# Kernel optimization log

Measured on AMD Instinct MI355X. Metric: run time of the kernel, lower is better.

## Reference

```python
import jax, jax.numpy as jnp
import numpy as np

EPS = 1e-7
K = 15      # kernel_size
CIN = 128
F = 256


def setup_inputs() -> dict:
    key = jax.random.key(0)
    k1, k2 = jax.random.split(key)
    x = jax.random.normal(k1, (32, 4096, CIN), dtype=jnp.float32)
    # glorot-uniform init then UnitNorm over axes (0,1) per filter, matching the constraint
    limit = np.sqrt(6.0 / (K * CIN + F))
    kernel = jax.random.uniform(k2, (K, CIN, F), dtype=jnp.float32, minval=-limit, maxval=limit)
    kernel = kernel / jnp.sqrt(jnp.sum(kernel * kernel, axis=(0, 1), keepdims=True) + 1e-12)
    scale = jnp.full((1, 1, 1), 10.0, dtype=jnp.float32)
    bias = jnp.zeros((F,), dtype=jnp.float32)
    return {"inputs": x, "kernel": kernel, "scale": scale, "bias": bias}


def reference(inputs, kernel, scale, bias):
    # dot-product conv: (B, L-K+1, F), VALID padding, stride 1
    dot = jax.lax.conv_general_dilated(
        inputs, kernel, window_strides=(1,), padding="VALID",
        dimension_numbers=("NWC", "WIO", "NWC"))
    # sliding sum-of-squares over window*channels. In the original this is a
    # conv1d with an all-ones (K,CIN,F) kernel, i.e. every filter sees the same
    # scalar sum -> compute it once via a cumsum box filter and broadcast.
    k = kernel.shape[0]
    sq = jnp.sum(inputs * inputs, axis=-1)                       # (B, L)
    cs = jnp.cumsum(jnp.pad(sq, ((0, 0), (1, 0))), axis=1)       # (B, L+1)
    win = cs[:, k:] - cs[:, :-k]                                 # (B, L-K+1)
    norm_x = jnp.sqrt(win + EPS)[..., None]                      # (B, L-K+1, 1)
    return scale * (dot / norm_x) + bias
```

## Files before the change

kernel.cpp:

```cpp
#include <hip/hip_runtime.h>
#include <hip/hip_bf16.h>
#include <stdint.h>

#define K_TAPS 15
#define CIN    128
#define F_OUT  256
#define LSEQ   4096
#define LOUT   (LSEQ - K_TAPS + 1)
#define BATCH  32

typedef __attribute__((ext_vector_type(8))) short bf16x8;
typedef __attribute__((ext_vector_type(4))) float f32x4;

typedef __attribute__((address_space(1))) const unsigned int gu32_t;
typedef __attribute__((address_space(3))) unsigned int su32_t;

__global__ void prep_w_kernel(const float* __restrict__ W,
                              unsigned short* __restrict__ Wp) {
  int idx = blockIdx.x * 256 + threadIdx.x;
  int f  = idx & 255;
  int kc = idx >> 8;
  int c  = kc & 127;
  int k  = kc >> 7;
  float w = W[idx];
  __hip_bfloat16 hb = __float2bfloat16(w);
  int ht = k * 2 + (c >> 6);
  int g  = (c >> 3) & 7;
  int c7 = c & 7;
  Wp[(((size_t)ht * 8 + g) * 256 + f) * 8 + c7] =
      *reinterpret_cast<unsigned short*>(&hb);
}

#define BM 128
#define BN 128
#define XROWS 144
#define XBYTES (XROWS * 256)
#define BBYTES 16384
#define NPHASE (K_TAPS * 2)

__global__ __launch_bounds__(256, 2) void conv_gemm_kernel(
    const float* __restrict__ x, const unsigned short* __restrict__ Wp,
    const float* __restrict__ scale, const float* __restrict__ bias,
    float* __restrict__ out)
{
  __shared__ __align__(16) char lds[XBYTES + 2 * BBYTES];
  __shared__ float sqs[XROWS];
  __shared__ float rns[BM];
  char* Xs = lds;
  char* Bs = lds + XBYTES;

  const int b     = blockIdx.y;
  const int mtile = blockIdx.x >> 1;
  const int ntile = blockIdx.x & 1;
  const int t0    = mtile * BM;
  const int n0    = ntile * BN;

  const int tx   = threadIdx.x;
  const int wid  = tx >> 6;
  const int lane = tx & 63;
  const int wm   = wid >> 1;
  const int wn   = wid & 1;

  const float scalev = scale[0];

  auto stageB = [&](int buf, int phase) {
    const char* src = (const char*)Wp + (size_t)phase * 32768;
    char* dst = Bs + buf * BBYTES;
    #pragma unroll
    for (int i = 0; i < 4; ++i) {
      int slot = i * 256 + tx;
      int g    = slot >> 7;
      int floc = slot & 127;
      __builtin_amdgcn_global_load_lds(
          (gu32_t*)(src + ((size_t)g * 256 + n0 + floc) * 16),
          (su32_t*)(dst + (size_t)slot * 16), 16, 0, 0);
    }
  };

  stageB(0, 0);

  {
    const int rloc = tx >> 4;
    const int g    = tx & 15;
    const float* xb = x + (long)b * LSEQ * CIN;
    #pragma unroll
    for (int it = 0; it < 9; ++it) {
      int row  = it * 16 + rloc;
      int grow = t0 + row;
      float v[8];
      if (grow < LSEQ) {
        const float4* p = (const float4*)(xb + (long)grow * CIN + g * 8);
        float4 a0 = p[0], a1 = p[1];
        v[0]=a0.x; v[1]=a0.y; v[2]=a0.z; v[3]=a0.w;
        v[4]=a1.x; v[5]=a1.y; v[6]=a1.z; v[7]=a1.w;
      } else {
        #pragma unroll
        for (int j = 0; j < 8; ++j) v[j] = 0.f;
      }
      float s = 0.f;
      union { unsigned short us[8]; int4 q; } pk;
      #pragma unroll
      for (int j = 0; j < 8; ++j) {
        s += v[j] * v[j];
        __hip_bfloat16 hb = __float2bfloat16(v[j]);
        pk.us[j] = *reinterpret_cast<unsigned short*>(&hb);
      }
      int slot = (g ^ row) & 15;
      *(int4*)(Xs + row * 256 + slot * 16) = pk.q;
      s += __shfl_xor(s, 1, 16);
      s += __shfl_xor(s, 2, 16);
      s += __shfl_xor(s, 4, 16);
      s += __shfl_xor(s, 8, 16);
      if (g == 0) sqs[row] = s;
    }
  }
  __syncthreads();

  if (tx < BM) {
    float wsum = 0.f;
    #pragma unroll
    for (int k = 0; k < K_TAPS; ++k) wsum += sqs[tx + k];
    rns[tx] = scalev / sqrtf(wsum + 1e-7f);
  }

  f32x4 acc[4][4] = {};

  const int klane = lane >> 4;
  const int rl    = lane & 15;
  const int arow0 = wm * 64;
  const int bcol0 = wn * 64;

  #pragma unroll 2
  for (int ph = 0; ph < NPHASE; ++ph) {
    const int buf = ph & 1;
    const int tap = ph >> 1;
    const int kk0 = (ph & 1) * 2;

    if (ph + 1 < NPHASE) stageB(buf ^ 1, ph + 1);

    bf16x8 af[2][4];
    #pragma unroll
    for (int j = 0; j < 2; ++j) {
      const int ga = (kk0 + j) * 4 + klane;
      #pragma unroll
      for (int mf = 0; mf < 4; ++mf) {
        int row  = arow0 + mf * 16 + rl + tap;
        int slot = (ga ^ row) & 15;
        af[j][mf] = *(const bf16x8*)(Xs + row * 256 + slot * 16);
      }
    }

    if (ph + 1 < NPHASE) {
      asm volatile("s_waitcnt vmcnt(4)" ::: "memory");
    } else {
      asm volatile("s_waitcnt vmcnt(0)" ::: "memory");
    }
    __builtin_amdgcn_s_barrier();

    const char* Bsc = Bs + buf * BBYTES;
    bf16x8 bfr[2][4];
    #pragma unroll
    for (int j = 0; j < 2; ++j) {
      const int gb = ((kk0 + j) & 1) * 4 + klane;
      #pragma unroll
      for (int nf = 0; nf < 4; ++nf) {
        int floc = bcol0 + nf * 16 + rl;
        bfr[j][nf] = *(const bf16x8*)(Bsc + ((size_t)gb * 128 + floc) * 16);
      }
    }

    __builtin_amdgcn_s_setprio(1);
    #pragma unroll
    for (int j = 0; j < 2; ++j)
      #pragma unroll
      for (int mf = 0; mf < 4; ++mf)
        #pragma unroll
        for (int nf = 0; nf < 4; ++nf)
          acc[mf][nf] = __builtin_amdgcn_mfma_f32_16x16x32_bf16(
              af[j][mf], bfr[j][nf], acc[mf][nf], 0, 0, 0);
    __builtin_amdgcn_s_setprio(0);

    asm volatile("s_waitcnt lgkmcnt(0)" ::: "memory");
    __builtin_amdgcn_s_barrier();
  }

  const int rgrp = lane >> 4;
  float biasv[4];
  #pragma unroll
  for (int nf = 0; nf < 4; ++nf) biasv[nf] = bias[n0 + bcol0 + nf * 16 + rl];
  float* ob = out + (long)b * LOUT * F_OUT;
  #pragma unroll
  for (int mf = 0; mf < 4; ++mf) {
    #pragma unroll
    for (int r = 0; r < 4; ++r) {
      int row = arow0 + mf * 16 + rgrp * 4 + r;
      int gt  = t0 + row;
      if (gt < LOUT) {
        float rv = rns[row];
        #pragma unroll
        for (int nf = 0; nf < 4; ++nf) {
          ob[(long)gt * F_OUT + n0 + bcol0 + nf * 16 + rl] =
              acc[mf][nf][r] * rv + biasv[nf];
        }
      }
    }
  }
}

extern "C" void kernel_launch(void* const* d_in, const int* in_sizes, int n_in,
                              void* d_out, int out_size, void* d_ws, size_t ws_size,
                              hipStream_t stream) {
  const float* x     = (const float*)d_in[0];
  const float* W     = (const float*)d_in[1];
  const float* scale = (const float*)d_in[2];
  const float* bias  = (const float*)d_in[3];
  float* out = (float*)d_out;

  unsigned short* Wp = (unsigned short*)d_ws;

  prep_w_kernel<<<1920, 256, 0, stream>>>(W, Wp);
  conv_gemm_kernel<<<dim3(64, BATCH), 256, 0, stream>>>(x, Wp, scale, bias, out);
}
```

Measured before the change: 158.9 us.

## Switch conv GEMM to 32x32x16 MFMA with new swizzled weight and LDS layouts

Replaces the 16x16x32 bf16 MFMA tiling with 32x32x16 MFMA tiles. Each wave now computes a 2x2 grid of 32x32 outputs, using two interleaved accumulator sets that are summed in the epilogue. The weight prep kernel now writes a per-filter, XOR-swizzled 64-channel layout so B can be staged with contiguous per-wave global-to-LDS copies, and the X swizzle is adjusted to match. The aim is fewer MFMA issues and fewer LDS fragment reads per phase. In exchange, the doubled accumulators raise register pressure and the new read patterns may cause LDS bank conflicts.

```diff
diff --git a/kernel.cpp b/kernel.cpp
--- a/kernel.cpp
+++ b/kernel.cpp
@@ -10,7 +10,7 @@
 #define BATCH  32
 
 typedef __attribute__((ext_vector_type(8))) short bf16x8;
-typedef __attribute__((ext_vector_type(4))) float f32x4;
+typedef __attribute__((ext_vector_type(16))) float f32x16;
 
 typedef __attribute__((address_space(1))) const unsigned int gu32_t;
 typedef __attribute__((address_space(3))) unsigned int su32_t;
@@ -24,10 +24,11 @@
   int k  = kc >> 7;
   float w = W[idx];
   __hip_bfloat16 hb = __float2bfloat16(w);
-  int ht = k * 2 + (c >> 6);
-  int g  = (c >> 3) & 7;
-  int c7 = c & 7;
-  Wp[(((size_t)ht * 8 + g) * 256 + f) * 8 + c7] =
+  int chalf = c >> 6;
+  int c6    = c & 63;
+  int slot  = ((c6 >> 3) ^ f) & 7;
+  int cp    = slot * 8 + (c & 7);
+  Wp[((size_t)(k * 2 + chalf) * 256 + f) * 64 + cp] =
       *reinterpret_cast<unsigned short*>(&hb);
 }
 
@@ -64,16 +65,16 @@
   const float scalev = scale[0];
 
   auto stageB = [&](int buf, int phase) {
-    const char* src = (const char*)Wp + (size_t)phase * 32768;
+    const char* src = (const char*)Wp + (size_t)phase * 32768
+                      + (size_t)n0 * 128;
     char* dst = Bs + buf * BBYTES;
+    int base = wid * 4096;
     #pragma unroll
     for (int i = 0; i < 4; ++i) {
-      int slot = i * 256 + tx;
-      int g    = slot >> 7;
-      int floc = slot & 127;
+      int off = base + i * 1024;
       __builtin_amdgcn_global_load_lds(
-          (gu32_t*)(src + ((size_t)g * 256 + n0 + floc) * 16),
-          (su32_t*)(dst + (size_t)slot * 16), 16, 0, 0);
+          (gu32_t*)(src + off + lane * 16),
+          (su32_t*)(dst + off), 16, 0, 0);
     }
   };
 
@@ -105,7 +106,7 @@
         __hip_bfloat16 hb = __float2bfloat16(v[j]);
         pk.us[j] = *reinterpret_cast<unsigned short*>(&hb);
       }
-      int slot = (g ^ row) & 15;
+      int slot = (g & 8) | ((g ^ row) & 7);
       *(int4*)(Xs + row * 256 + slot * 16) = pk.q;
       s += __shfl_xor(s, 1, 16);
       s += __shfl_xor(s, 2, 16);
@@ -123,30 +124,30 @@
     rns[tx] = scalev / sqrtf(wsum + 1e-7f);
   }
 
-  f32x4 acc[4][4] = {};
-
-  const int klane = lane >> 4;
-  const int rl    = lane & 15;
+  f32x16 acc[2][2][2] = {};
+
+  const int l31   = lane & 31;
+  const int khalf = lane >> 5;
   const int arow0 = wm * 64;
   const int bcol0 = wn * 64;
 
   #pragma unroll 2
   for (int ph = 0; ph < NPHASE; ++ph) {
-    const int buf = ph & 1;
-    const int tap = ph >> 1;
-    const int kk0 = (ph & 1) * 2;
+    const int buf    = ph & 1;
+    const int tap    = ph >> 1;
+    const int chalf8 = (ph & 1) * 8;
 
     if (ph + 1 < NPHASE) stageB(buf ^ 1, ph + 1);
 
-    bf16x8 af[2][4];
-    #pragma unroll
-    for (int j = 0; j < 2; ++j) {
-      const int ga = (kk0 + j) * 4 + klane;
-      #pragma unroll
-      for (int mf = 0; mf < 4; ++mf) {
-        int row  = arow0 + mf * 16 + rl + tap;
-        int slot = (ga ^ row) & 15;
-        af[j][mf] = *(const bf16x8*)(Xs + row * 256 + slot * 16);
+    bf16x8 af[4][2];
+    #pragma unroll
+    for (int s = 0; s < 4; ++s) {
+      const int ga = chalf8 + 2 * s + khalf;
+      #pragma unroll
+      for (int wfm = 0; wfm < 2; ++wfm) {
+        int row  = arow0 + wfm * 32 + l31 + tap;
+        int slot = (ga & 8) | ((ga ^ row) & 7);
+        af[s][wfm] = *(const bf16x8*)(Xs + row * 256 + slot * 16);
       }
     }
 
@@ -158,49 +159,51 @@
     __builtin_amdgcn_s_barrier();
 
     const char* Bsc = Bs + buf * BBYTES;
-    bf16x8 bfr[2][4];
-    #pragma unroll
-    for (int j = 0; j < 2; ++j) {
-      const int gb = ((kk0 + j) & 1) * 4 + klane;
-      #pragma unroll
-      for (int nf = 0; nf < 4; ++nf) {
-        int floc = bcol0 + nf * 16 + rl;
-        bfr[j][nf] = *(const bf16x8*)(Bsc + ((size_t)gb * 128 + floc) * 16);
+    bf16x8 bfr[4][2];
+    #pragma unroll
+    for (int s = 0; s < 4; ++s) {
+      const int gb = 2 * s + khalf;
+      #pragma unroll
+      for (int wfn = 0; wfn < 2; ++wfn) {
+        int fc   = bcol0 + wfn * 32 + l31;
+        int slot = (gb ^ fc) & 7;
+        bfr[s][wfn] = *(const bf16x8*)(Bsc + fc * 128 + slot * 16);
       }
     }
 
     __builtin_amdgcn_s_setprio(1);
     #pragma unroll
-    for (int j = 0; j < 2; ++j)
-      #pragma unroll
-      for (int mf = 0; mf < 4; ++mf)
+    for (int s = 0; s < 4; ++s)
+      #pragma unroll
+      for (int wfm = 0; wfm < 2; ++wfm)
         #pragma unroll
-        for (int nf = 0; nf < 4; ++nf)
-          acc[mf][nf] = __builtin_amdgcn_mfma_f32_16x16x32_bf16(
-              af[j][mf], bfr[j][nf], acc[mf][nf], 0, 0, 0);
+        for (int wfn = 0; wfn < 2; ++wfn)
+          acc[s & 1][wfm][wfn] = __builtin_amdgcn_mfma_f32_32x32x16_bf16(
+              af[s][wfm], bfr[s][wfn], acc[s & 1][wfm][wfn], 0, 0, 0);
     __builtin_amdgcn_s_setprio(0);
 
     asm volatile("s_waitcnt lgkmcnt(0)" ::: "memory");
     __builtin_amdgcn_s_barrier();
   }
 
-  const int rgrp = lane >> 4;
-  float biasv[4];
+  float* ob = out + (long)b * LOUT * F_OUT;
+  float biasv[2];
   #pragma unroll
-  for (int nf = 0; nf < 4; ++nf) biasv[nf] = bias[n0 + bcol0 + nf * 16 + rl];
-  float* ob = out + (long)b * LOUT * F_OUT;
+  for (int wfn = 0; wfn < 2; ++wfn)
+    biasv[wfn] = bias[n0 + bcol0 + wfn * 32 + l31];
   #pragma unroll
-  for (int mf = 0; mf < 4; ++mf) {
-    #pragma unroll
-    for (int r = 0; r < 4; ++r) {
-      int row = arow0 + mf * 16 + rgrp * 4 + r;
-      int gt  = t0 + row;
+  for (int wfm = 0; wfm < 2; ++wfm) {
+    #pragma unroll
+    for (int reg = 0; reg < 16; ++reg) {
+      int rloc = arow0 + wfm * 32 + (reg & 3) + 8 * (reg >> 2) + 4 * khalf;
+      int gt   = t0 + rloc;
       if (gt < LOUT) {
-        float rv = rns[row];
+        float rv = rns[rloc];
         #pragma unroll
-        for (int nf = 0; nf < 4; ++nf) {
-          ob[(long)gt * F_OUT + n0 + bcol0 + nf * 16 + rl] =
-              acc[mf][nf][r] * rv + biasv[nf];
+        for (int wfn = 0; wfn < 2; ++wfn) {
+          float v = acc[0][wfm][wfn][reg] + acc[1][wfm][wfn][reg];
+          ob[(long)gt * F_OUT + n0 + bcol0 + wfn * 32 + l31] =
+              v * rv + biasv[wfn];
         }
       }
     }
```

Result: slower. 184.4 us (+16.0%).

## Enlarge conv GEMM tile to 256x256 with 512 threads and swizzled weight layout

Applied to the files above, without the earlier changes.

Each block now covers all 256 filters and 256 output positions with 8 waves, instead of a 128x128 tile with 4 waves. This removes the duplicate staging and bf16 conversion of the input tile across the two filter halves, and shrinks the relative cost of the 14-row halo. The weight prep kernel writes an XOR-swizzled per-filter layout, so B tiles are staged as contiguous wave-sized chunks and read from LDS with fewer bank conflicts. The cost is about 132KB of LDS per block, which likely allows only one block per CU, plus heavier register use (128 accumulators per lane). The grid is also cut to 512 blocks, which reduces load balancing and latency hiding.

```diff
diff --git a/kernel.cpp b/kernel.cpp
--- a/kernel.cpp
+++ b/kernel.cpp
@@ -24,21 +24,22 @@
   int k  = kc >> 7;
   float w = W[idx];
   __hip_bfloat16 hb = __float2bfloat16(w);
-  int ht = k * 2 + (c >> 6);
-  int g  = (c >> 3) & 7;
-  int c7 = c & 7;
-  Wp[(((size_t)ht * 8 + g) * 256 + f) * 8 + c7] =
+  int chalf = c >> 6;
+  int c6    = c & 63;
+  int slot  = ((c6 >> 3) ^ f) & 7;
+  int cp    = slot * 8 + (c & 7);
+  Wp[((size_t)(k * 2 + chalf) * 256 + f) * 64 + cp] =
       *reinterpret_cast<unsigned short*>(&hb);
 }
 
-#define BM 128
-#define BN 128
-#define XROWS 144
+#define BM 256
+#define BN 256
+#define XROWS 272
 #define XBYTES (XROWS * 256)
-#define BBYTES 16384
+#define BBYTES 32768
 #define NPHASE (K_TAPS * 2)
 
-__global__ __launch_bounds__(256, 2) void conv_gemm_kernel(
+__global__ __launch_bounds__(512, 2) void conv_gemm_kernel(
     const float* __restrict__ x, const unsigned short* __restrict__ Wp,
     const float* __restrict__ scale, const float* __restrict__ bias,
     float* __restrict__ out)
@@ -49,17 +50,14 @@
   char* Xs = lds;
   char* Bs = lds + XBYTES;
 
-  const int b     = blockIdx.y;
-  const int mtile = blockIdx.x >> 1;
-  const int ntile = blockIdx.x & 1;
-  const int t0    = mtile * BM;
-  const int n0    = ntile * BN;
+  const int b  = blockIdx.y;
+  const int t0 = blockIdx.x * BM;
 
   const int tx   = threadIdx.x;
   const int wid  = tx >> 6;
   const int lane = tx & 63;
-  const int wm   = wid >> 1;
-  const int wn   = wid & 1;
+  const int wm   = wid >> 2;
+  const int wn   = wid & 3;
 
   const float scalev = scale[0];
 
@@ -68,12 +66,10 @@
     char* dst = Bs + buf * BBYTES;
     #pragma unroll
     for (int i = 0; i < 4; ++i) {
-      int slot = i * 256 + tx;
-      int g    = slot >> 7;
-      int floc = slot & 127;
+      int off = i * 8192 + wid * 1024;
       __builtin_amdgcn_global_load_lds(
-          (gu32_t*)(src + ((size_t)g * 256 + n0 + floc) * 16),
-          (su32_t*)(dst + (size_t)slot * 16), 16, 0, 0);
+          (gu32_t*)(src + off + lane * 16),
+          (su32_t*)(dst + off), 16, 0, 0);
     }
   };
 
@@ -85,33 +81,35 @@
     const float* xb = x + (long)b * LSEQ * CIN;
     #pragma unroll
     for (int it = 0; it < 9; ++it) {
-      int row  = it * 16 + rloc;
+      int row  = it * 32 + rloc;
       int grow = t0 + row;
-      float v[8];
-      if (grow < LSEQ) {
-        const float4* p = (const float4*)(xb + (long)grow * CIN + g * 8);
-        float4 a0 = p[0], a1 = p[1];
-        v[0]=a0.x; v[1]=a0.y; v[2]=a0.z; v[3]=a0.w;
-        v[4]=a1.x; v[5]=a1.y; v[6]=a1.z; v[7]=a1.w;
-      } else {
+      if (row < XROWS) {
+        float v[8];
+        if (grow < LSEQ) {
+          const float4* p = (const float4*)(xb + (long)grow * CIN + g * 8);
+          float4 a0 = p[0], a1 = p[1];
+          v[0]=a0.x; v[1]=a0.y; v[2]=a0.z; v[3]=a0.w;
+          v[4]=a1.x; v[5]=a1.y; v[6]=a1.z; v[7]=a1.w;
+        } else {
+          #pragma unroll
+          for (int j = 0; j < 8; ++j) v[j] = 0.f;
+        }
+        float s = 0.f;
+        union { unsigned short us[8]; int4 q; } pk;
         #pragma unroll
-        for (int j = 0; j < 8; ++j) v[j] = 0.f;
-      }
-      float s = 0.f;
-      union { unsigned short us[8]; int4 q; } pk;
-      #pragma unroll
-      for (int j = 0; j < 8; ++j) {
-        s += v[j] * v[j];
-        __hip_bfloat16 hb = __float2bfloat16(v[j]);
-        pk.us[j] = *reinterpret_cast<unsigned short*>(&hb);
-      }
-      int slot = (g ^ row) & 15;
-      *(int4*)(Xs + row * 256 + slot * 16) = pk.q;
-      s += __shfl_xor(s, 1, 16);
-      s += __shfl_xor(s, 2, 16);
-      s += __shfl_xor(s, 4, 16);
-      s += __shfl_xor(s, 8, 16);
-      if (g == 0) sqs[row] = s;
+        for (int j = 0; j < 8; ++j) {
+          s += v[j] * v[j];
+          __hip_bfloat16 hb = __float2bfloat16(v[j]);
+          pk.us[j] = *reinterpret_cast<unsigned short*>(&hb);
+        }
+        int slot = (g & 8) | ((g ^ row) & 7);
+        *(int4*)(Xs + row * 256 + slot * 16) = pk.q;
+        s += __shfl_xor(s, 1, 16);
+        s += __shfl_xor(s, 2, 16);
+        s += __shfl_xor(s, 4, 16);
+        s += __shfl_xor(s, 8, 16);
+        if (g == 0) sqs[row] = s;
+      }
     }
   }
   __syncthreads();
@@ -123,11 +121,11 @@
     rns[tx] = scalev / sqrtf(wsum + 1e-7f);
   }
 
-  f32x4 acc[4][4] = {};
+  f32x4 acc[8][4] = {};
 
   const int klane = lane >> 4;
   const int rl    = lane & 15;
-  const int arow0 = wm * 64;
+  const int arow0 = wm * 128;
   const int bcol0 = wn * 64;
 
   #pragma unroll 2
@@ -138,14 +136,14 @@
 
     if (ph + 1 < NPHASE) stageB(buf ^ 1, ph + 1);
 
-    bf16x8 af[2][4];
+    bf16x8 af[2][8];
     #pragma unroll
     for (int j = 0; j < 2; ++j) {
       const int ga = (kk0 + j) * 4 + klane;
       #pragma unroll
-      for (int mf = 0; mf < 4; ++mf) {
+      for (int mf = 0; mf < 8; ++mf) {
         int row  = arow0 + mf * 16 + rl + tap;
-        int slot = (ga ^ row) & 15;
+        int slot = (ga & 8) | ((ga ^ row) & 7);
         af[j][mf] = *(const bf16x8*)(Xs + row * 256 + slot * 16);
       }
     }
@@ -158,27 +156,25 @@
     __builtin_amdgcn_s_barrier();
 
     const char* Bsc = Bs + buf * BBYTES;
-    bf16x8 bfr[2][4];
     #pragma unroll
     for (int j = 0; j < 2; ++j) {
       const int gb = ((kk0 + j) & 1) * 4 + klane;
+      bf16x8 bfr[4];
       #pragma unroll
       for (int nf = 0; nf < 4; ++nf) {
-        int floc = bcol0 + nf * 16 + rl;
-        bfr[j][nf] = *(const bf16x8*)(Bsc + ((size_t)gb * 128 + floc) * 16);
-      }
-    }
-
-    __builtin_amdgcn_s_setprio(1);
-    #pragma unroll
-    for (int j = 0; j < 2; ++j)
+        int fc   = bcol0 + nf * 16 + rl;
+        int slot = (gb ^ fc) & 7;
+        bfr[nf] = *(const bf16x8*)(Bsc + fc * 128 + slot * 16);
+      }
+      __builtin_amdgcn_s_setprio(1);
       #pragma unroll
-      for (int mf = 0; mf < 4; ++mf)
+      for (int mf = 0; mf < 8; ++mf)
         #pragma unroll
         for (int nf = 0; nf < 4; ++nf)
           acc[mf][nf] = __builtin_amdgcn_mfma_f32_16x16x32_bf16(
-              af[j][mf], bfr[j][nf], acc[mf][nf], 0, 0, 0);
-    __builtin_amdgcn_s_setprio(0);
+              af[j][mf], bfr[nf], acc[mf][nf], 0, 0, 0);
+      __builtin_amdgcn_s_setprio(0);
+    }
 
     asm volatile("s_waitcnt lgkmcnt(0)" ::: "memory");
     __builtin_amdgcn_s_barrier();
@@ -187,10 +183,10 @@
   const int rgrp = lane >> 4;
   float biasv[4];
   #pragma unroll
-  for (int nf = 0; nf < 4; ++nf) biasv[nf] = bias[n0 + bcol0 + nf * 16 + rl];
+  for (int nf = 0; nf < 4; ++nf) biasv[nf] = bias[bcol0 + nf * 16 + rl];
   float* ob = out + (long)b * LOUT * F_OUT;
   #pragma unroll
-  for (int mf = 0; mf < 4; ++mf) {
+  for (int mf = 0; mf < 8; ++mf) {
     #pragma unroll
     for (int r = 0; r < 4; ++r) {
       int row = arow0 + mf * 16 + rgrp * 4 + r;
@@ -199,7 +195,7 @@
         float rv = rns[row];
         #pragma unroll
         for (int nf = 0; nf < 4; ++nf) {
-          ob[(long)gt * F_OUT + n0 + bcol0 + nf * 16 + rl] =
+          ob[(long)gt * F_OUT + bcol0 + nf * 16 + rl] =
               acc[mf][nf][r] * rv + biasv[nf];
         }
       }
@@ -219,5 +215,5 @@
   unsigned short* Wp = (unsigned short*)d_ws;
 
   prep_w_kernel<<<1920, 256, 0, stream>>>(W, Wp);
-  conv_gemm_kernel<<<dim3(64, BATCH), 256, 0, stream>>>(x, Wp, scale, bias, out);
+  conv_gemm_kernel<<<dim3(16, BATCH), 512, 0, stream>>>(x, Wp, scale, bias, out);
 }
```

Result: no change. 156.4 us (-1.6%).

## Repack weights F-major with XOR swizzle for contiguous B staging and fewer bank conflicts

Applied to the files above, without the earlier changes.

Changes the prepacked weight layout so that each filter holds 64 contiguous channels, with an XOR swizzle on 16-byte slots keyed by the filter index. The B tile then becomes one contiguous 16 KB chunk, so each wave stages 4 KB with lane-contiguous global_load_lds transfers. The X tile swizzle is narrowed to 8 slots within each 128-byte half, and the B fragment reads use the matching swizzle. The goal is more coalesced global loads and fewer LDS bank conflicts on the B reads, though the narrower X swizzle could change the conflict pattern on A reads.

```diff
diff --git a/kernel.cpp b/kernel.cpp
--- a/kernel.cpp
+++ b/kernel.cpp
@@ -24,10 +24,11 @@
   int k  = kc >> 7;
   float w = W[idx];
   __hip_bfloat16 hb = __float2bfloat16(w);
-  int ht = k * 2 + (c >> 6);
-  int g  = (c >> 3) & 7;
-  int c7 = c & 7;
-  Wp[(((size_t)ht * 8 + g) * 256 + f) * 8 + c7] =
+  int chalf = c >> 6;
+  int c6    = c & 63;
+  int slot  = ((c6 >> 3) ^ f) & 7;
+  int cp    = slot * 8 + (c & 7);
+  Wp[((size_t)(k * 2 + chalf) * 256 + f) * 64 + cp] =
       *reinterpret_cast<unsigned short*>(&hb);
 }
 
@@ -64,16 +65,16 @@
   const float scalev = scale[0];
 
   auto stageB = [&](int buf, int phase) {
-    const char* src = (const char*)Wp + (size_t)phase * 32768;
+    const char* src = (const char*)Wp + (size_t)phase * 32768
+                      + (size_t)n0 * 128;
     char* dst = Bs + buf * BBYTES;
+    int base = wid * 4096;
     #pragma unroll
     for (int i = 0; i < 4; ++i) {
-      int slot = i * 256 + tx;
-      int g    = slot >> 7;
-      int floc = slot & 127;
+      int off = base + i * 1024;
       __builtin_amdgcn_global_load_lds(
-          (gu32_t*)(src + ((size_t)g * 256 + n0 + floc) * 16),
-          (su32_t*)(dst + (size_t)slot * 16), 16, 0, 0);
+          (gu32_t*)(src + off + lane * 16),
+          (su32_t*)(dst + off), 16, 0, 0);
     }
   };
 
@@ -105,7 +106,7 @@
         __hip_bfloat16 hb = __float2bfloat16(v[j]);
         pk.us[j] = *reinterpret_cast<unsigned short*>(&hb);
       }
-      int slot = (g ^ row) & 15;
+      int slot = (g & 8) | ((g ^ row) & 7);
       *(int4*)(Xs + row * 256 + slot * 16) = pk.q;
       s += __shfl_xor(s, 1, 16);
       s += __shfl_xor(s, 2, 16);
@@ -145,7 +146,7 @@
       #pragma unroll
       for (int mf = 0; mf < 4; ++mf) {
         int row  = arow0 + mf * 16 + rl + tap;
-        int slot = (ga ^ row) & 15;
+        int slot = (ga & 8) | ((ga ^ row) & 7);
         af[j][mf] = *(const bf16x8*)(Xs + row * 256 + slot * 16);
       }
     }
@@ -164,8 +165,9 @@
       const int gb = ((kk0 + j) & 1) * 4 + klane;
       #pragma unroll
       for (int nf = 0; nf < 4; ++nf) {
-        int floc = bcol0 + nf * 16 + rl;
-        bfr[j][nf] = *(const bf16x8*)(Bsc + ((size_t)gb * 128 + floc) * 16);
+        int fc   = bcol0 + nf * 16 + rl;
+        int slot = (gb ^ fc) & 7;
+        bfr[j][nf] = *(const bf16x8*)(Bsc + fc * 128 + slot * 16);
       }
     }
 
```

New measurement: 155.5 us. 2.2% less time.
